# Optimization experiments

Hardware: AMD Instinct MI355X
Metric: run time of the kernel (lower is better)

Reference implementation:

```python
import jax, jax.numpy as jnp
import numpy as np

RANK = 16
ALPHA = 32
SCALE = ALPHA / RANK


def setup_inputs() -> dict:
    key = jax.random.key(0)
    ks = jax.random.split(key, 4)
    B_, S, D, K = 4, 2048, 4096, 4096
    x = jax.random.normal(ks[0], (B_, S, D), dtype=jnp.float32)
    W = jax.random.normal(ks[1], (K, D), dtype=jnp.float32) * 0.02  # torch Linear weight [out,in]
    bias = jax.random.normal(ks[2], (K,), dtype=jnp.float32) * 0.02
    B = jnp.zeros((D, RANK), dtype=jnp.float32)  # LoRA B init to zeros
    A = jax.random.normal(ks[3], (RANK, K), dtype=jnp.float32)
    return {"x": x, "W": W, "bias": bias, "B": B, "A": A}


def reference(x, W, bias, B, A):
    # base linear: x @ W^T + bias
    base = jnp.einsum("bsd,kd->bsk", x, W) + bias
    # low-rank path: scale * (x @ B) @ A
    lora = SCALE * jnp.einsum("bsr,rk->bsk", jnp.einsum("bsd,dr->bsr", x, B), A)
    return base + lora
```

## Files before the change

### kernel.cpp

```cpp
#include <hip/hip_runtime.h>

typedef unsigned short u16;
typedef __attribute__((ext_vector_type(4))) unsigned short u16x4;
typedef __attribute__((ext_vector_type(8))) unsigned short u16x8;
typedef __attribute__((ext_vector_type(8))) short bf16x8;
typedef __attribute__((ext_vector_type(4))) float f32x4;

#define LORA_SCALE 2.0f

__device__ __forceinline__ u16 f2bf(float f) {
  unsigned u = __builtin_bit_cast(unsigned, f);
  u += 0x7FFFu + ((u >> 16) & 1u);
  return (u16)(u >> 16);
}

#define GLOAD16(g, l) __builtin_amdgcn_global_load_lds(                        \
    (const __attribute__((address_space(1))) void*)(g),                        \
    (__attribute__((address_space(3))) void*)(l), 16, 0, 0)

__global__ __launch_bounds__(256) void make_weff(
    const float* __restrict__ W, const float* __restrict__ B,
    const float* __restrict__ A, u16* __restrict__ Wb)
{
  __shared__ float sA[16][64];
  const int n0 = (blockIdx.x >> 4) * 64;
  const int k0 = (blockIdx.x & 15) * 256;
  const int t  = threadIdx.x;

  {
    const int r = t >> 4;
    const int j = (t & 15) * 4;
    const float4 v = *(const float4*)(A + (size_t)r * 4096 + n0 + j);
    sA[r][j + 0] = LORA_SCALE * v.x;
    sA[r][j + 1] = LORA_SCALE * v.y;
    sA[r][j + 2] = LORA_SCALE * v.z;
    sA[r][j + 3] = LORA_SCALE * v.w;
  }
  __syncthreads();

  const int tn = t >> 6;
  const int tk = t & 63;

  float bv[64];
  const float4* pb = (const float4*)(B + (size_t)(k0 + tk * 4) * 16);
#pragma unroll
  for (int q = 0; q < 16; ++q) {
    float4 v = pb[q];
    bv[q * 4 + 0] = v.x; bv[q * 4 + 1] = v.y;
    bv[q * 4 + 2] = v.z; bv[q * 4 + 3] = v.w;
  }

  for (int i = 0; i < 16; ++i) {
    const int n = n0 + tn * 16 + i;
    const float4 w4 = *(const float4*)(W + (size_t)n * 4096 + k0 + tk * 4);
    float acc[4] = {w4.x, w4.y, w4.z, w4.w};
#pragma unroll
    for (int j = 0; j < 4; ++j)
#pragma unroll
      for (int r = 0; r < 16; ++r)
        acc[j] += bv[j * 16 + r] * sA[r][tn * 16 + i];
    u16x4 o;
    o[0] = f2bf(acc[0]); o[1] = f2bf(acc[1]);
    o[2] = f2bf(acc[2]); o[3] = f2bf(acc[3]);
    *(u16x4*)(Wb + (size_t)n * 4096 + k0 + tk * 4) = o;
  }
}

__global__ __launch_bounds__(256) void cvt_x_kernel(
    const float* __restrict__ x, u16* __restrict__ xb, long n)
{
  long i0 = ((long)blockIdx.x * blockDim.x + threadIdx.x) * 8;
  long stride = (long)gridDim.x * blockDim.x * 8;
  for (long i = i0; i < n; i += stride) {
    float4 a = *(const float4*)(x + i);
    float4 b = *(const float4*)(x + i + 4);
    u16x8 o;
    o[0] = f2bf(a.x); o[1] = f2bf(a.y); o[2] = f2bf(a.z); o[3] = f2bf(a.w);
    o[4] = f2bf(b.x); o[5] = f2bf(b.y); o[6] = f2bf(b.z); o[7] = f2bf(b.w);
    *(u16x8*)(xb + i) = o;
  }
}

#define BM 128
#define BN 128
#define BKK 64

__global__ __launch_bounds__(256) void gemm_bias(
    const u16* __restrict__ Xb, const u16* __restrict__ Wb,
    const float* __restrict__ bias, float* __restrict__ out)
{
  const int K = 4096, N = 4096;
  __shared__ u16 sA[BM][BKK];
  __shared__ u16 sB[BN][BKK];

  const int t  = threadIdx.x;
  const int l  = t & 63;
  const int w  = t >> 6;
  const int wr = w >> 1;
  const int wc = w & 1;

  const int ntn = N / BN;
  const int tm = blockIdx.x / ntn, tn = blockIdx.x % ntn;
  const int m0 = tm * BM, n0 = tn * BN;

  const int srow = t >> 3;
  const int scol = (t & 7) * 8;
  const u16* gA = Xb + (size_t)(m0 + srow) * K + scol;
  const u16* gB = Wb + (size_t)(n0 + srow) * K + scol;
  char* lA = (char*)(&sA[0][0]) + t * 16;
  char* lB = (char*)(&sB[0][0]) + t * 16;

  f32x4 acc[4][4];
#pragma unroll
  for (int i = 0; i < 4; ++i)
#pragma unroll
    for (int j = 0; j < 4; ++j) acc[i][j] = (f32x4){0.f, 0.f, 0.f, 0.f};

  const int fr = l & 15;
  const int fq = l >> 4;

  for (int kt = 0; kt < K; kt += BKK) {
#pragma unroll
    for (int c = 0; c < 4; ++c) {
      GLOAD16(gA + (size_t)(c * 32) * K + kt, lA + c * 4096);
      GLOAD16(gB + (size_t)(c * 32) * K + kt, lB + c * 4096);
    }
    asm volatile("s_waitcnt vmcnt(0)" ::: "memory");
    __syncthreads();

#pragma unroll
    for (int ks = 0; ks < BKK; ks += 32) {
      bf16x8 af[4], bfr[4];
#pragma unroll
      for (int mi = 0; mi < 4; ++mi)
        af[mi] = *(const bf16x8*)&sA[wr * 64 + mi * 16 + fr][ks + fq * 8];
#pragma unroll
      for (int nj = 0; nj < 4; ++nj)
        bfr[nj] = *(const bf16x8*)&sB[wc * 64 + nj * 16 + fr][ks + fq * 8];
#pragma unroll
      for (int mi = 0; mi < 4; ++mi)
#pragma unroll
        for (int nj = 0; nj < 4; ++nj)
          acc[mi][nj] = __builtin_amdgcn_mfma_f32_16x16x32_bf16(
              af[mi], bfr[nj], acc[mi][nj], 0, 0, 0);
    }
    __syncthreads();
  }

  float bvals[4];
#pragma unroll
  for (int nj = 0; nj < 4; ++nj) bvals[nj] = bias[n0 + wc * 64 + nj * 16 + fr];

#pragma unroll
  for (int mi = 0; mi < 4; ++mi) {
#pragma unroll
    for (int i = 0; i < 4; ++i) {
      const int m = m0 + wr * 64 + mi * 16 + fq * 4 + i;
      float* orow = out + (size_t)m * N + n0 + wc * 64 + fr;
#pragma unroll
      for (int nj = 0; nj < 4; ++nj)
        orow[nj * 16] = acc[mi][nj][i] + bvals[nj];
    }
  }
}

extern "C" void kernel_launch(void* const* d_in, const int* in_sizes, int n_in,
                              void* d_out, int out_size, void* d_ws, size_t ws_size,
                              hipStream_t stream) {
  const float* x    = (const float*)d_in[0];
  const float* W    = (const float*)d_in[1];
  const float* bias = (const float*)d_in[2];
  const float* B    = (const float*)d_in[3];
  const float* A    = (const float*)d_in[4];
  float* out = (float*)d_out;

  u16* Xb = (u16*)d_ws;
  u16* Wb = Xb + (size_t)8192 * 4096;

  make_weff<<<dim3(1024), dim3(256), 0, stream>>>(W, B, A, Wb);
  cvt_x_kernel<<<dim3(2048), dim3(256), 0, stream>>>(x, Xb, (long)8192 * 4096);
  gemm_bias<<<dim3(2048), dim3(256), 0, stream>>>(Xb, Wb, bias, out);
}
```

Before: 590.8 us.

## Replace GEMM with 256x256-tile triple-buffered pipelined MFMA kernel

Replaces the 128x128 single-buffered bf16 GEMM with a 256x256 tile kernel that uses 512 threads. The K dimension is staged through a three-buffer LDS ring with split A/B prefetch two tiles ahead, partial vmcnt waits, XOR-swizzled LDS addressing to avoid bank conflicts, s_setprio around MFMA blocks, and a block-index swizzle for L2 locality. The goal is to hide global load latency behind MFMA work and raise arithmetic intensity per LDS byte. It adds 96KB of LDS, so occupancy is lower, and it brings register pressure from 32 accumulators plus subtle barrier-ordering risks.

```diff
diff --git a/kernel.cpp b/kernel.cpp
--- a/kernel.cpp
+++ b/kernel.cpp
@@ -81,87 +81,117 @@
   }
 }
 
-#define BM 128
-#define BN 128
-#define BKK 64
-
-__global__ __launch_bounds__(256) void gemm_bias(
+__global__ __launch_bounds__(512, 2) void gemm256(
     const u16* __restrict__ Xb, const u16* __restrict__ Wb,
     const float* __restrict__ bias, float* __restrict__ out)
 {
-  const int K = 4096, N = 4096;
-  __shared__ u16 sA[BM][BKK];
-  __shared__ u16 sB[BN][BKK];
-
-  const int t  = threadIdx.x;
-  const int l  = t & 63;
-  const int w  = t >> 6;
-  const int wr = w >> 1;
-  const int wc = w & 1;
-
-  const int ntn = N / BN;
-  const int tm = blockIdx.x / ntn, tn = blockIdx.x % ntn;
-  const int m0 = tm * BM, n0 = tn * BN;
-
-  const int srow = t >> 3;
-  const int scol = (t & 7) * 8;
-  const u16* gA = Xb + (size_t)(m0 + srow) * K + scol;
-  const u16* gB = Wb + (size_t)(n0 + srow) * K + scol;
-  char* lA = (char*)(&sA[0][0]) + t * 16;
-  char* lB = (char*)(&sB[0][0]) + t * 16;
-
-  f32x4 acc[4][4];
-#pragma unroll
-  for (int i = 0; i < 4; ++i)
+  constexpr int K = 4096, N = 4096;
+  constexpr int NT = K / 32;
+  __shared__ char lds[3 * 32768];
+
+  const int t = threadIdx.x;
+  const int w = t >> 6, l = t & 63;
+  const int wave_m = w >> 2, wave_n = w & 3;
+
+  const int bid = blockIdx.x;
+  const int swz = (bid & 7) * 64 + (bid >> 3);
+  const int tm = swz >> 4, tn = swz & 15;
+  const int m0 = tm * 256, n0 = tn * 256;
+
+  const int lrow = l >> 2;
+  const int lch  = ((l & 3) ^ ((l >> 3) & 3)) * 8;
+  const u16* gAs = Xb + (size_t)(m0 + w * 16 + lrow) * K + lch;
+  const u16* gBs = Wb + (size_t)(n0 + w * 16 + lrow) * K + lch;
+  char* ldsw = lds + w * 1024;
+
+#define STAGE_A(tt, bb) do {                                                   \
+    GLOAD16(gAs + (size_t)(tt) * 32,                  ldsw + (bb) * 32768);    \
+    GLOAD16(gAs + (size_t)(tt) * 32 + 128 * (size_t)K, ldsw + (bb) * 32768 + 8192); \
+  } while (0)
+#define STAGE_B(tt, bb) do {                                                   \
+    GLOAD16(gBs + (size_t)(tt) * 32,                  ldsw + (bb) * 32768 + 16384); \
+    GLOAD16(gBs + (size_t)(tt) * 32 + 128 * (size_t)K, ldsw + (bb) * 32768 + 16384 + 8192); \
+  } while (0)
+
+  const int fr = l & 15, fq = l >> 4;
+  const int coff = (fq ^ ((fr >> 1) & 3)) << 4;
+  const char* pa0 = lds + (wave_m * 128 + fr) * 64 + coff;
+  const char* pb0 = lds + 16384 + (wave_n * 64 + fr) * 64 + coff;
+
+  f32x4 acc[8][4];
+#pragma unroll
+  for (int i = 0; i < 8; ++i)
 #pragma unroll
     for (int j = 0; j < 4; ++j) acc[i][j] = (f32x4){0.f, 0.f, 0.f, 0.f};
 
-  const int fr = l & 15;
-  const int fq = l >> 4;
-
-  for (int kt = 0; kt < K; kt += BKK) {
-#pragma unroll
-    for (int c = 0; c < 4; ++c) {
-      GLOAD16(gA + (size_t)(c * 32) * K + kt, lA + c * 4096);
-      GLOAD16(gB + (size_t)(c * 32) * K + kt, lB + c * 4096);
-    }
-    asm volatile("s_waitcnt vmcnt(0)" ::: "memory");
-    __syncthreads();
-
-#pragma unroll
-    for (int ks = 0; ks < BKK; ks += 32) {
-      bf16x8 af[4], bfr[4];
-#pragma unroll
-      for (int mi = 0; mi < 4; ++mi)
-        af[mi] = *(const bf16x8*)&sA[wr * 64 + mi * 16 + fr][ks + fq * 8];
+  STAGE_A(0, 0); STAGE_B(0, 0);
+  STAGE_A(1, 1); STAGE_B(1, 1);
+  asm volatile("s_waitcnt vmcnt(4)" ::: "memory");
+  __builtin_amdgcn_s_barrier();
+
+  int b = 0;
+  for (int tt = 0; tt < NT; ++tt) {
+    const char* pa = pa0 + b * 32768;
+    const char* pb = pb0 + b * 32768;
+    const int bs = (b == 2) ? 0 : b + 1;
+    const int b2 = (b >= 1) ? b - 1 : 2;
+
+    bf16x8 bf[4], af[4];
+#pragma unroll
+    for (int nj = 0; nj < 4; ++nj)
+      bf[nj] = *(const bf16x8*)(pb + nj * 1024);
+#pragma unroll
+    for (int mi = 0; mi < 4; ++mi)
+      af[mi] = *(const bf16x8*)(pa + mi * 1024);
+    if (tt + 2 < NT) STAGE_A(tt + 2, b2);
+    __builtin_amdgcn_s_barrier();
+    __builtin_amdgcn_s_setprio(1);
+#pragma unroll
+    for (int mi = 0; mi < 4; ++mi)
 #pragma unroll
       for (int nj = 0; nj < 4; ++nj)
-        bfr[nj] = *(const bf16x8*)&sB[wc * 64 + nj * 16 + fr][ks + fq * 8];
-#pragma unroll
-      for (int mi = 0; mi < 4; ++mi)
+        acc[mi][nj] = __builtin_amdgcn_mfma_f32_16x16x32_bf16(
+            af[mi], bf[nj], acc[mi][nj], 0, 0, 0);
+    __builtin_amdgcn_s_setprio(0);
+    __builtin_amdgcn_s_barrier();
+
+#pragma unroll
+    for (int mi = 0; mi < 4; ++mi)
+      af[mi] = *(const bf16x8*)(pa + 4096 + mi * 1024);
+    if (tt + 2 < NT) STAGE_B(tt + 2, b2);
+    __builtin_amdgcn_s_barrier();
+    __builtin_amdgcn_s_setprio(1);
+#pragma unroll
+    for (int mi = 0; mi < 4; ++mi)
+#pragma unroll
+      for (int nj = 0; nj < 4; ++nj)
+        acc[4 + mi][nj] = __builtin_amdgcn_mfma_f32_16x16x32_bf16(
+            af[mi], bf[nj], acc[4 + mi][nj], 0, 0, 0);
+    __builtin_amdgcn_s_setprio(0);
+    if (tt + 2 < NT) { asm volatile("s_waitcnt vmcnt(4)" ::: "memory"); }
+    else             { asm volatile("s_waitcnt vmcnt(0)" ::: "memory"); }
+    __builtin_amdgcn_s_barrier();
+
+    b = bs;
+  }
+
+  float bvals[4];
+#pragma unroll
+  for (int nj = 0; nj < 4; ++nj)
+    bvals[nj] = bias[n0 + wave_n * 64 + nj * 16 + fr];
+
+#pragma unroll
+  for (int ph = 0; ph < 2; ++ph)
+#pragma unroll
+    for (int mi = 0; mi < 4; ++mi)
+#pragma unroll
+      for (int i = 0; i < 4; ++i) {
+        const int m = m0 + wave_m * 128 + ph * 64 + mi * 16 + fq * 4 + i;
+        float* orow = out + (size_t)m * N + n0 + wave_n * 64 + fr;
 #pragma unroll
         for (int nj = 0; nj < 4; ++nj)
-          acc[mi][nj] = __builtin_amdgcn_mfma_f32_16x16x32_bf16(
-              af[mi], bfr[nj], acc[mi][nj], 0, 0, 0);
-    }
-    __syncthreads();
-  }
-
-  float bvals[4];
-#pragma unroll
-  for (int nj = 0; nj < 4; ++nj) bvals[nj] = bias[n0 + wc * 64 + nj * 16 + fr];
-
-#pragma unroll
-  for (int mi = 0; mi < 4; ++mi) {
-#pragma unroll
-    for (int i = 0; i < 4; ++i) {
-      const int m = m0 + wr * 64 + mi * 16 + fq * 4 + i;
-      float* orow = out + (size_t)m * N + n0 + wc * 64 + fr;
-#pragma unroll
-      for (int nj = 0; nj < 4; ++nj)
-        orow[nj * 16] = acc[mi][nj][i] + bvals[nj];
-    }
-  }
+          orow[nj * 16] = acc[ph * 4 + mi][nj][i] + bvals[nj];
+      }
 }
 
 extern "C" void kernel_launch(void* const* d_in, const int* in_sizes, int n_in,
@@ -179,5 +209,5 @@
 
   make_weff<<<dim3(1024), dim3(256), 0, stream>>>(W, B, A, Wb);
   cvt_x_kernel<<<dim3(2048), dim3(256), 0, stream>>>(x, Xb, (long)8192 * 4096);
-  gemm_bias<<<dim3(2048), dim3(256), 0, stream>>>(Xb, Wb, bias, out);
-}
+  gemm256<<<dim3(512), dim3(512), 0, stream>>>(Xb, Wb, bias, out);
+}
```

After: 516.9 us. -12.5%, faster.
